# Performance work log

Measured on AMD Instinct MI355X. Metric: run time of the kernel, lower is better.

## Reference

```python
import jax, jax.numpy as jnp
import numpy as np

MIN_NORM = 1e-15
PROJ_EPS = 4e-3  # HGCN float32 boundary eps
C = 1.0          # curvature (all layers)
N_BRANCH = 4


def artanh(x):
    return jnp.arctanh(jnp.clip(x, -1.0 + 1e-7, 1.0 - 1e-7))


def _norm(x):
    return jnp.clip(jnp.linalg.norm(x, axis=-1, keepdims=True), MIN_NORM)


def proj(x, c):
    n = _norm(x)
    maxn = (1.0 - PROJ_EPS) / jnp.sqrt(c)
    return jnp.where(n > maxn, x / n * maxn, x)


def expmap0(u, c):
    sc = jnp.sqrt(c)
    n = _norm(u)
    return jnp.tanh(sc * n) * u / (sc * n)


def logmap0(p, c):
    sc = jnp.sqrt(c)
    n = _norm(p)
    return artanh(sc * n) * p / (sc * n)


def mobius_add(x, y, c):
    x2 = jnp.sum(x * x, -1, keepdims=True)
    y2 = jnp.sum(y * y, -1, keepdims=True)
    xy = jnp.sum(x * y, -1, keepdims=True)
    num = (1.0 + 2.0 * c * xy + c * y2) * x + (1.0 - c * x2) * y
    den = 1.0 + 2.0 * c * xy + c * c * x2 * y2
    return num / jnp.clip(den, MIN_NORM)


def mobius_matvec(W, x, c):
    sc = jnp.sqrt(c)
    xn = _norm(x)
    mx = x @ W.T
    mxn = _norm(mx)
    res = jnp.tanh(mxn / xn * artanh(sc * xn)) * mx / (mxn * sc)
    zero = jnp.all(mx == 0, axis=-1, keepdims=True)
    return jnp.where(zero, jnp.zeros((), x.dtype), res)


def mobius_mulscaler(r, x, c):
    sc = jnp.sqrt(c)
    xn = _norm(x)
    return jnp.tanh(r * artanh(sc * xn)) * x / (xn * sc)


def spmm(src, dst, w, xt, n):
    # out[i] = sum_{e: dst[e]=i} w[e] * xt[src[e]]
    return jax.ops.segment_sum(w[:, None] * xt[src], dst, num_segments=n)


def hgc_layer(h, W, b, src, dst, w, n):
    # HypLinear (dropout=0)
    h = proj(mobius_matvec(W, h, C), C)
    hb = proj(expmap0(b[None, :], C), C)
    h = proj(mobius_add(h, hb, C), C)
    # HypAgg: sparse propagation in tangent space
    st = spmm(src, dst, w, logmap0(h, C), n)
    h = proj(expmap0(st, C), C)
    # HypAct (relu)
    return proj(expmap0(jax.nn.relu(logmap0(h, C)), C), C)


def encode(x, W0, b0, W1, b1, src, dst, w, n):
    h = proj(expmap0(x, C), C)  # proj_tan0 is identity on Poincare ball
    h = hgc_layer(h, W0, b0, src, dst, w, n)
    h = hgc_layer(h, W1, b1, src, dst, w, n)
    return h


def setup_inputs() -> dict:
    key = jax.random.key(0)
    ks = jax.random.split(key, 8)
    N, F_IN, HID, DIM, E = 50000, 128, 128, 64, 1600000
    x = jax.random.normal(ks[0], (N, F_IN), jnp.float32)
    edge_src = jax.random.randint(ks[1], (E,), 0, N, jnp.int32)
    edge_dst = jax.random.randint(ks[2], (E,), 0, N, jnp.int32)
    # positive, roughly row-normalized edge weights (avg degree 32)
    edge_w = jax.random.uniform(ks[3], (N_BRANCH, E), jnp.float32) / 32.0
    W0 = jax.random.normal(ks[4], (N_BRANCH, HID, F_IN), jnp.float32) * 0.05
    b0 = jax.random.normal(ks[5], (N_BRANCH, HID), jnp.float32) * 0.01
    W1 = jax.random.normal(ks[6], (N_BRANCH, DIM, HID), jnp.float32) * 0.05
    b1 = jax.random.normal(ks[7], (N_BRANCH, DIM), jnp.float32) * 0.01
    return {"x": x, "edge_src": edge_src, "edge_dst": edge_dst, "edge_w": edge_w,
            "W0": W0, "b0": b0, "W1": W1, "b1": b1}


def reference(x, edge_src, edge_dst, edge_w, W0, b0, W1, b1):
    n = x.shape[0]
    # 4 directional-proximity branches (d_i, d_o, n_i, n_o); fixed small loop
    branches = [encode(x, W0[i], b0[i], W1[i], b1[i], edge_src, edge_dst, edge_w[i], n)
                for i in range(N_BRANCH)]
    # Mobius-weighted (scalar 1/8) combination, left-to-right mobius_add chain
    target = mobius_mulscaler(0.125, branches[0], C)
    for br in branches[1:]:
        target = mobius_add(target, mobius_mulscaler(0.125, br, C), C)
    feat = jnp.stack(branches + [target], axis=1)  # [N, 5, dim]
    # HypAttnAgg (use_att=False) with row-normalized per-node star adjacency:
    # target row of each 5-block = mean of the 5 tangent vectors
    agg = logmap0(feat, C).mean(axis=1)            # [N, dim]
    return proj(expmap0(agg, C), C)
```

## Files before the change

### kernel.cpp

```cpp
#include <hip/hip_runtime.h>
#include <math.h>

#define MAXN_P 0.996f

typedef unsigned short bfraw;
typedef __attribute__((ext_vector_type(8))) short bf16x8;
typedef __attribute__((ext_vector_type(4))) float f32x4;

__device__ __forceinline__ float wred(float v){
  #pragma unroll
  for(int o=32;o>0;o>>=1) v += __shfl_xor(v,o,64);
  return v;
}
template<int W>
__device__ __forceinline__ float gredw(float v){
  #pragma unroll
  for(int o=W/2;o>0;o>>=1) v += __shfl_xor(v,o,64);
  return v;
}
__device__ __forceinline__ float artanh_c(float x){
  x = fminf(fmaxf(x, -1.0f+1e-7f), 1.0f-1e-7f);
  return atanhf(x);
}
__device__ __forceinline__ float sel4(float4 w, int g){
  float ab = (g&1) ? w.y : w.x;
  float cd = (g&1) ? w.w : w.z;
  return (g&2) ? cd : ab;
}
__device__ __forceinline__ bfraw f2bf(float f){
  unsigned u = __float_as_uint(f);
  unsigned r = (u + 0x7fffu + ((u>>16)&1u)) >> 16;
  return (bfraw)r;
}
__device__ __forceinline__ float bflo(unsigned u){ return __uint_as_float(u<<16); }
__device__ __forceinline__ float bfhi(unsigned u){ return __uint_as_float(u & 0xffff0000u); }

__device__ __forceinline__ void acc8(float* a, float w, uint4 u){
  a[0]=fmaf(w, bflo(u.x), a[0]); a[1]=fmaf(w, bfhi(u.x), a[1]);
  a[2]=fmaf(w, bflo(u.y), a[2]); a[3]=fmaf(w, bfhi(u.y), a[3]);
  a[4]=fmaf(w, bflo(u.z), a[4]); a[5]=fmaf(w, bfhi(u.z), a[5]);
  a[6]=fmaf(w, bflo(u.w), a[6]); a[7]=fmaf(w, bfhi(u.w), a[7]);
}
__device__ __forceinline__ void acc4(float* a, float w, uint2 u){
  a[0]=fmaf(w, bflo(u.x), a[0]); a[1]=fmaf(w, bfhi(u.x), a[1]);
  a[2]=fmaf(w, bflo(u.y), a[2]); a[3]=fmaf(w, bfhi(u.y), a[3]);
}

template<int W, int K>
__device__ __forceinline__ float postK(const float* u, float* h){
  float ss = 0.f;
  #pragma unroll
  for(int k=0;k<K;k++) ss += u[k]*u[k];
  ss = gredw<W>(ss);
  float un = fmaxf(sqrtf(ss), 1e-15f);
  float t1 = tanhf(un);
  float sc = t1/un;
  float pn = t1;
  if (pn > MAXN_P){ sc *= MAXN_P/pn; pn = MAXN_P; }
  float ln = fmaxf(pn, 1e-15f);
  float m = sc * (artanh_c(ln)/ln);
  float v[K]; float vs = 0.f;
  #pragma unroll
  for(int k=0;k<K;k++){ v[k] = fmaxf(u[k]*m, 0.f); vs += v[k]*v[k]; }
  vs = gredw<W>(vs);
  float vn = fmaxf(sqrtf(vs), 1e-15f);
  float t2 = tanhf(vn);
  float qs = t2/vn;
  float qn = t2;
  if (qn > MAXN_P){ qs *= MAXN_P/qn; qn = MAXN_P; }
  #pragma unroll
  for(int k=0;k<K;k++) h[k] = v[k]*qs;
  return qn;
}

__global__ void k_hist(const int* __restrict__ dst, int* __restrict__ cnt, int E){
  int e = blockIdx.x*blockDim.x + threadIdx.x;
  if (e < E) atomicAdd(&cnt[dst[e]], 1);
}

__global__ void k_scan(const int* __restrict__ cnt, int* __restrict__ rowptr,
                       int* __restrict__ cursor, int N){
  __shared__ int sh[1024];
  int t = threadIdx.x;
  int chunk = (N + 1023) / 1024;
  int b = t*chunk;
  int e = b + chunk; if (e > N) e = N;
  int s = 0;
  for(int i=b;i<e && i<N;i++) s += cnt[i];
  sh[t] = s;
  __syncthreads();
  for(int off=1; off<1024; off<<=1){
    int add = (t>=off) ? sh[t-off] : 0;
    __syncthreads();
    sh[t] += add;
    __syncthreads();
  }
  int run = (t==0) ? 0 : sh[t-1];
  for(int i=b;i<e && i<N;i++){
    rowptr[i] = run; cursor[i] = run; run += cnt[i];
  }
  if (t == 1023) rowptr[N] = run;
}

__global__ void k_fill(const int* __restrict__ src, const int* __restrict__ dst,
                       const float* __restrict__ ew, int E,
                       int* __restrict__ cursor, int* __restrict__ srcs,
                       float4* __restrict__ wq){
  int e = blockIdx.x*blockDim.x + threadIdx.x;
  if (e >= E) return;
  int d = dst[e];
  int pos = atomicAdd(&cursor[d], 1);
  srcs[pos] = src[e];
  wq[pos] = make_float4(ew[e], ew[(size_t)E + e], ew[2*(size_t)E + e], ew[3*(size_t)E + e]);
}

__global__ void k_exp0(const float* __restrict__ x, bfraw* __restrict__ h0,
                       float* __restrict__ n0, int N){
  int wid = (blockIdx.x*blockDim.x + threadIdx.x)>>6;
  int lane = threadIdx.x & 63;
  if (wid >= N) return;
  const float* r = x + (size_t)wid*128;
  float u0 = r[lane], u1 = r[lane+64];
  float ss = wred(u0*u0 + u1*u1);
  float un = fmaxf(sqrtf(ss), 1e-15f);
  float tn = tanhf(un);
  float sc = tn/un;
  float pn = tn;
  if (pn > MAXN_P){ sc *= MAXN_P/pn; pn = MAXN_P; }
  h0[(size_t)wid*128 + lane]      = f2bf(u0*sc);
  h0[(size_t)wid*128 + lane + 64] = f2bf(u1*sc);
  if (lane == 0) n0[wid] = pn;
}

__global__ void k_hb(const float* __restrict__ b0, const float* __restrict__ b1,
                     float* __restrict__ hb0, float* __restrict__ hb1,
                     int HID, int DIM){
  int bl = blockIdx.x;
  int lane = threadIdx.x;
  int layer = bl >> 2, br = bl & 3;
  int D = layer ? DIM : HID;
  const float* b = layer ? (b1 + (size_t)br*DIM) : (b0 + (size_t)br*HID);
  float* o       = layer ? (hb1 + (size_t)br*DIM) : (hb0 + (size_t)br*HID);
  float v0 = (lane < D) ? b[lane] : 0.f;
  float v1 = (lane+64 < D) ? b[lane+64] : 0.f;
  float ss = wred(v0*v0 + v1*v1);
  float n = fmaxf(sqrtf(ss), 1e-15f);
  float tn = tanhf(n);
  float sc = tn/n;
  if (tn > MAXN_P) sc *= MAXN_P/tn;
  if (lane < D)    o[lane]    = v0*sc;
  if (lane+64 < D) o[lane+64] = v1*sc;
}

__global__ void k_w2bf(const float* __restrict__ a, bfraw* __restrict__ o, int n){
  int i = blockIdx.x*blockDim.x + threadIdx.x;
  if (i < n) o[i] = f2bf(a[i]);
}

template<int CT>
__global__ __launch_bounds__(256) void k_gemm_fused(
    const bfraw* __restrict__ Abase, int lda, int abroff,
    const bfraw* __restrict__ Wb,
    const float* __restrict__ nin, int nstride, int nbroff,
    const float* __restrict__ hball,
    bfraw* __restrict__ xt,
    int M)
{
  constexpr int BN = CT*16;
  __shared__ bfraw tile[64*BN];
  int br = blockIdx.z;
  const bfraw* A = Abase + (size_t)br*abroff;
  const bfraw* W = Wb + (size_t)br*BN*128;
  const float* hb = hball + (size_t)br*BN;
  int rb = blockIdx.x*64;
  int t = threadIdx.x;
  int wave = t>>6, lane = t&63;
  int cl = lane&15, grp = lane>>4;

  int rowA = rb + wave*16 + cl;
  bf16x8 afr[4];
  bf16x8 zf = {0,0,0,0,0,0,0,0};
  #pragma unroll
  for(int ks=0;ks<4;ks++){
    if (rowA < M) afr[ks] = *(const bf16x8*)(A + (size_t)rowA*lda + ks*32 + grp*8);
    else          afr[ks] = zf;
  }
  f32x4 acc[CT];
  #pragma unroll
  for(int ct=0;ct<CT;ct++) acc[ct] = f32x4{0.f,0.f,0.f,0.f};
  #pragma unroll
  for(int ct=0;ct<CT;ct++){
    #pragma unroll
    for(int ks=0;ks<4;ks++){
      bf16x8 bfr = *(const bf16x8*)(W + (size_t)(ct*16+cl)*128 + ks*32 + grp*8);
      acc[ct] = __builtin_amdgcn_mfma_f32_16x16x32_bf16(afr[ks], bfr, acc[ct], 0,0,0);
    }
  }
  float hv[CT]; float hb2 = 0.f;
  #pragma unroll
  for(int ct=0;ct<CT;ct++){ hv[ct] = hb[cl+16*ct]; hb2 += hv[ct]*hv[ct]; }
  hb2 = gredw<16>(hb2);
  #pragma unroll
  for(int j=0;j<4;j++){
    int rloc = wave*16 + grp*4 + j;
    int node = rb + rloc;
    bool v = node < M;
    float m[CT]; float ss = 0.f;
    #pragma unroll
    for(int ct=0;ct<CT;ct++){ m[ct] = acc[ct][j]; ss += m[ct]*m[ct]; }
    ss = gredw<16>(ss);
    float mxn_raw = sqrtf(ss);
    float mxn = fmaxf(mxn_raw, 1e-15f);
    float xn = fmaxf(v ? nin[(size_t)node*nstride + br*nbroff] : 1.f, 1e-15f);
    float th = tanhf(mxn/xn * artanh_c(xn));
    float hs = (mxn_raw > 0.f) ? th/mxn : 0.f;
    float hn = (mxn_raw > 0.f) ? th : 0.f;
    if (hn > MAXN_P){ hs *= MAXN_P/hn; hn = MAXN_P; }
    float h[CT]; float xy = 0.f, x2 = 0.f;
    #pragma unroll
    for(int ct=0;ct<CT;ct++){ h[ct] = m[ct]*hs; xy += h[ct]*hv[ct]; x2 += h[ct]*h[ct]; }
    xy = gredw<16>(xy); x2 = gredw<16>(x2);
    float c1 = 1.f + 2.f*xy + hb2;
    float c2 = 1.f - x2;
    float den = fmaxf(1.f + 2.f*xy + x2*hb2, 1e-15f);
    float a[CT]; float as = 0.f;
    #pragma unroll
    for(int ct=0;ct<CT;ct++){ a[ct] = (c1*h[ct] + c2*hv[ct])/den; as += a[ct]*a[ct]; }
    as = gredw<16>(as);
    float an = fmaxf(sqrtf(as), 1e-15f);
    float s2 = 1.f;
    if (an > MAXN_P){ s2 = MAXN_P/an; an = MAXN_P; }
    float ls = artanh_c(an)/an * s2;
    #pragma unroll
    for(int ct=0;ct<CT;ct++) tile[rloc*BN + cl + 16*ct] = f2bf(a[ct]*ls);
  }
  __syncthreads();
  constexpr int IT = (64*BN)/(256*8);
  #pragma unroll
  for(int i=0;i<IT;i++){
    int flat = (t + i*256)*8;
    int row = flat/BN, col = flat%BN;
    int node = rb + row;
    if (node < M)
      *(uint4*)(xt + ((size_t)node*4 + br)*BN + col) = *(const uint4*)(tile + row*BN + col);
  }
}

__global__ __launch_bounds__(256) void k_spmm_l0(const int* __restrict__ rowptr,
                        const int* __restrict__ srcs, const float4* __restrict__ wq,
                        const bfraw* __restrict__ xt,
                        bfraw* __restrict__ hout, float* __restrict__ n4, int N){
  int wid = (blockIdx.x*blockDim.x + threadIdx.x)>>6;
  int lane = threadIdx.x & 63;
  if (wid >= N) return;
  int g = lane>>4;
  float acc[8] = {0,0,0,0,0,0,0,0};
  int p0 = rowptr[wid], p1 = rowptr[wid+1];
  int p = p0;
  for (; p+4 <= p1; p += 4){
    int s0 = srcs[p], s1 = srcs[p+1], s2 = srcs[p+2], s3 = srcs[p+3];
    float4 w0 = wq[p], w1 = wq[p+1], w2 = wq[p+2], w3 = wq[p+3];
    uint4 u0 = *((const uint4*)(xt + (size_t)s0*512) + lane);
    uint4 u1 = *((const uint4*)(xt + (size_t)s1*512) + lane);
    uint4 u2 = *((const uint4*)(xt + (size_t)s2*512) + lane);
    uint4 u3 = *((const uint4*)(xt + (size_t)s3*512) + lane);
    acc8(acc, sel4(w0,g), u0);
    acc8(acc, sel4(w1,g), u1);
    acc8(acc, sel4(w2,g), u2);
    acc8(acc, sel4(w3,g), u3);
  }
  for (; p < p1; ++p){
    int s0 = srcs[p];
    float4 w0 = wq[p];
    uint4 u0 = *((const uint4*)(xt + (size_t)s0*512) + lane);
    acc8(acc, sel4(w0,g), u0);
  }
  float h[8];
  float qn = postK<16,8>(acc, h);
  uint4 o;
  o.x = (unsigned)f2bf(h[0]) | ((unsigned)f2bf(h[1])<<16);
  o.y = (unsigned)f2bf(h[2]) | ((unsigned)f2bf(h[3])<<16);
  o.z = (unsigned)f2bf(h[4]) | ((unsigned)f2bf(h[5])<<16);
  o.w = (unsigned)f2bf(h[6]) | ((unsigned)f2bf(h[7])<<16);
  *((uint4*)(hout + (size_t)wid*512) + lane) = o;
  if ((lane&15)==0) n4[(size_t)wid*4 + g] = qn;
}

__global__ __launch_bounds__(256) void k_spmm_l1(const int* __restrict__ rowptr,
                        const int* __restrict__ srcs, const float4* __restrict__ wq,
                        const bfraw* __restrict__ xt,
                        float* __restrict__ out, int N){
  int wid = (blockIdx.x*blockDim.x + threadIdx.x)>>6;
  int lane = threadIdx.x & 63;
  if (wid >= N) return;
  int g = lane>>4;
  int slot = lane & 15;
  float acc[4] = {0,0,0,0};
  int p0 = rowptr[wid], p1 = rowptr[wid+1];
  int p = p0;
  for (; p+4 <= p1; p += 4){
    int s0 = srcs[p], s1 = srcs[p+1], s2 = srcs[p+2], s3 = srcs[p+3];
    float4 w0 = wq[p], w1 = wq[p+1], w2 = wq[p+2], w3 = wq[p+3];
    uint2 u0 = *((const uint2*)(xt + (size_t)s0*256) + lane);
    uint2 u1 = *((const uint2*)(xt + (size_t)s1*256) + lane);
    uint2 u2 = *((const uint2*)(xt + (size_t)s2*256) + lane);
    uint2 u3 = *((const uint2*)(xt + (size_t)s3*256) + lane);
    acc4(acc, sel4(w0,g), u0);
    acc4(acc, sel4(w1,g), u1);
    acc4(acc, sel4(w2,g), u2);
    acc4(acc, sel4(w3,g), u3);
  }
  for (; p < p1; ++p){
    int s0 = srcs[p];
    float4 w0 = wq[p];
    uint2 u0 = *((const uint2*)(xt + (size_t)s0*256) + lane);
    acc4(acc, sel4(w0,g), u0);
  }
  float hv[4];
  float qn = postK<16,4>(acc, hv);
  float xk[4][4]; float qk[4];
  #pragma unroll
  for(int k=0;k<4;k++){
    #pragma unroll
    for(int j=0;j<4;j++) xk[k][j] = __shfl(hv[j], slot + 16*k, 64);
    qk[k] = __shfl(qn, 16*k, 64);
  }
  float xn0 = fmaxf(qk[0], 1e-15f);
  float s0 = tanhf(0.125f*artanh_c(xn0))/xn0;
  float t[4] = {s0*xk[0][0], s0*xk[0][1], s0*xk[0][2], s0*xk[0][3]};
  #pragma unroll
  for(int k=1;k<4;k++){
    float yn = fmaxf(qk[k], 1e-15f);
    float sy = tanhf(0.125f*artanh_c(yn))/yn;
    float y[4] = {sy*xk[k][0], sy*xk[k][1], sy*xk[k][2], sy*xk[k][3]};
    float dx=0.f, dy=0.f, dxy=0.f;
    #pragma unroll
    for(int j=0;j<4;j++){ dx += t[j]*t[j]; dy += y[j]*y[j]; dxy += t[j]*y[j]; }
    float x2 = gredw<16>(dx);
    float y2 = gredw<16>(dy);
    float xy = gredw<16>(dxy);
    float c1 = 1.f + 2.f*xy + y2;
    float c2 = 1.f - x2;
    float den = fmaxf(1.f + 2.f*xy + x2*y2, 1e-15f);
    #pragma unroll
    for(int j=0;j<4;j++) t[j] = (c1*t[j] + c2*y[j])/den;
  }
  float s[4] = {0,0,0,0};
  #pragma unroll
  for(int k=0;k<4;k++){
    float nk = fmaxf(qk[k], 1e-15f);
    float lk = artanh_c(nk)/nk;
    #pragma unroll
    for(int j=0;j<4;j++) s[j] = fmaf(lk, xk[k][j], s[j]);
  }
  float dt = 0.f;
  #pragma unroll
  for(int j=0;j<4;j++) dt += t[j]*t[j];
  float tn = fmaxf(sqrtf(gredw<16>(dt)), 1e-15f);
  float lt = artanh_c(tn)/tn;
  #pragma unroll
  for(int j=0;j<4;j++) s[j] = 0.2f*fmaf(lt, t[j], s[j]);
  float ds = 0.f;
  #pragma unroll
  for(int j=0;j<4;j++) ds += s[j]*s[j];
  float an = fmaxf(sqrtf(gredw<16>(ds)), 1e-15f);
  float on = tanhf(an);
  float osc = on/an;
  if (on > MAXN_P) osc *= MAXN_P/on;
  if (g == 0)
    *(float4*)(out + (size_t)wid*64 + 4*slot) =
      make_float4(s[0]*osc, s[1]*osc, s[2]*osc, s[3]*osc);
}

extern "C" void kernel_launch(void* const* d_in, const int* in_sizes, int n_in,
                              void* d_out, int out_size, void* d_ws, size_t ws_size,
                              hipStream_t stream){
  const float* x   = (const float*)d_in[0];
  const int*   src = (const int*)d_in[1];
  const int*   dst = (const int*)d_in[2];
  const float* ew  = (const float*)d_in[3];
  const float* W0  = (const float*)d_in[4];
  const float* b0  = (const float*)d_in[5];
  const float* W1  = (const float*)d_in[6];
  const float* b1  = (const float*)d_in[7];
  float* out = (float*)d_out;

  const int FIN = 128;
  int N = in_sizes[0]/FIN;
  int E = in_sizes[1];
  int HID = in_sizes[5]/4;
  int DIM = in_sizes[7]/4;

  char* ws = (char*)d_ws;
  size_t off = 0;
  auto alloc = [&](size_t bytes)->char*{
    char* p = ws + off;
    off += (bytes + 255) & ~(size_t)255;
    return p;
  };
  bfraw* h4b    = (bfraw*)alloc((size_t)N*4*FIN*2);
  bfraw* xtb    = (bfraw*)alloc((size_t)N*4*FIN*2);
  float* n0     = (float*)alloc((size_t)N*4);
  float* n4     = (float*)alloc((size_t)N*16);
  int*   rowptr = (int*)alloc((size_t)(N+1)*4);
  int*   cnt    = (int*)alloc((size_t)N*4);
  int*   cursor = (int*)alloc((size_t)N*4);
  int*   srcs   = (int*)alloc((size_t)E*4);
  float4* wq    = (float4*)alloc((size_t)E*16);
  float* hb0    = (float*)alloc((size_t)4*HID*4);
  float* hb1    = (float*)alloc((size_t)4*DIM*4);
  bfraw* w0b    = (bfraw*)alloc((size_t)4*HID*FIN*2);
  bfraw* w1b    = (bfraw*)alloc((size_t)4*DIM*HID*2);
  (void)ws_size; (void)n_in; (void)out_size;

  bfraw* h0 = h4b;

  int rowBlocks  = (N + 3)/4;

  hipMemsetAsync(cnt, 0, (size_t)N*4, stream);
  k_hist<<<(E+255)/256, 256, 0, stream>>>(dst, cnt, E);
  k_scan<<<1, 1024, 0, stream>>>(cnt, rowptr, cursor, N);
  k_fill<<<(E+255)/256, 256, 0, stream>>>(src, dst, ew, E, cursor, srcs, wq);

  k_exp0<<<rowBlocks, 256, 0, stream>>>(x, h0, n0, N);
  k_hb<<<8, 64, 0, stream>>>(b0, b1, hb0, hb1, HID, DIM);
  k_w2bf<<<(4*HID*FIN+255)/256, 256, 0, stream>>>(W0, w0b, 4*HID*FIN);
  k_w2bf<<<(4*DIM*HID+255)/256, 256, 0, stream>>>(W1, w1b, 4*DIM*HID);

  k_gemm_fused<8><<<dim3((N+63)/64, 1, 4), 256, 0, stream>>>(
      h0, FIN, 0, w0b, n0, 1, 0, hb0, xtb, N);
  k_spmm_l0<<<rowBlocks, 256, 0, stream>>>(rowptr, srcs, wq, xtb, h4b, n4, N);

  k_gemm_fused<4><<<dim3((N+63)/64, 1, 4), 256, 0, stream>>>(
      h4b, 4*HID, HID, w1b, n4, 4, 1, hb1, xtb, N);
  k_spmm_l1<<<rowBlocks, 256, 0, stream>>>(rowptr, srcs, wq, xtb, out, N);
}
```

Measured before the change: 812.9 us.

## Pack edge weights to fp16 and process two edges per wave in layer-1 SpMM

Edge weights for the four branches are stored as packed fp16 (8 bytes per edge) instead of float4 (16 bytes), halving the weight traffic in both SpMM passes and in the fill kernel. The layer-1 SpMM now splits the wave into two halves, each handling a different edge with 16-byte loads, and combines the halves with a cross-half shuffle. The Mobius combination epilogue is restructured to match the 8-lane groups. The cost is reduced edge-weight precision and a more complex lane mapping.

New measurement: 832.1 us. 1.02x slower.

```diff
diff --git a/kernel.cpp b/kernel.cpp
--- a/kernel.cpp
+++ b/kernel.cpp
@@ -21,11 +21,6 @@
 __device__ __forceinline__ float artanh_c(float x){
   x = fminf(fmaxf(x, -1.0f+1e-7f), 1.0f-1e-7f);
   return atanhf(x);
-}
-__device__ __forceinline__ float sel4(float4 w, int g){
-  float ab = (g&1) ? w.y : w.x;
-  float cd = (g&1) ? w.w : w.z;
-  return (g&2) ? cd : ab;
 }
 __device__ __forceinline__ bfraw f2bf(float f){
   unsigned u = __float_as_uint(f);
@@ -34,16 +29,24 @@
 }
 __device__ __forceinline__ float bflo(unsigned u){ return __uint_as_float(u<<16); }
 __device__ __forceinline__ float bfhi(unsigned u){ return __uint_as_float(u & 0xffff0000u); }
+
+__device__ __forceinline__ unsigned short f2h(float f){
+  _Float16 x = (_Float16)f; unsigned short h; __builtin_memcpy(&h, &x, 2); return h;
+}
+__device__ __forceinline__ float h2f(unsigned short h){
+  _Float16 f; __builtin_memcpy(&f, &h, 2); return (float)f;
+}
+__device__ __forceinline__ float wsel(uint2 w, bool g1, bool g2){
+  unsigned word = g2 ? w.y : w.x;
+  unsigned hu = g1 ? (word>>16) : (word & 0xffffu);
+  return h2f((unsigned short)hu);
+}
 
 __device__ __forceinline__ void acc8(float* a, float w, uint4 u){
   a[0]=fmaf(w, bflo(u.x), a[0]); a[1]=fmaf(w, bfhi(u.x), a[1]);
   a[2]=fmaf(w, bflo(u.y), a[2]); a[3]=fmaf(w, bfhi(u.y), a[3]);
   a[4]=fmaf(w, bflo(u.z), a[4]); a[5]=fmaf(w, bfhi(u.z), a[5]);
   a[6]=fmaf(w, bflo(u.w), a[6]); a[7]=fmaf(w, bfhi(u.w), a[7]);
-}
-__device__ __forceinline__ void acc4(float* a, float w, uint2 u){
-  a[0]=fmaf(w, bflo(u.x), a[0]); a[1]=fmaf(w, bfhi(u.x), a[1]);
-  a[2]=fmaf(w, bflo(u.y), a[2]); a[3]=fmaf(w, bfhi(u.y), a[3]);
 }
 
 template<int W, int K>
@@ -105,13 +108,17 @@
 __global__ void k_fill(const int* __restrict__ src, const int* __restrict__ dst,
                        const float* __restrict__ ew, int E,
                        int* __restrict__ cursor, int* __restrict__ srcs,
-                       float4* __restrict__ wq){
+                       uint2* __restrict__ wq2){
   int e = blockIdx.x*blockDim.x + threadIdx.x;
   if (e >= E) return;
   int d = dst[e];
   int pos = atomicAdd(&cursor[d], 1);
   srcs[pos] = src[e];
-  wq[pos] = make_float4(ew[e], ew[(size_t)E + e], ew[2*(size_t)E + e], ew[3*(size_t)E + e]);
+  unsigned h0 = f2h(ew[e]);
+  unsigned h1 = f2h(ew[(size_t)E + e]);
+  unsigned h2 = f2h(ew[2*(size_t)E + e]);
+  unsigned h3 = f2h(ew[3*(size_t)E + e]);
+  wq2[pos] = make_uint2(h0 | (h1<<16), h2 | (h3<<16));
 }
 
 __global__ void k_exp0(const float* __restrict__ x, bfraw* __restrict__ h0,
@@ -247,33 +254,34 @@
 }
 
 __global__ __launch_bounds__(256) void k_spmm_l0(const int* __restrict__ rowptr,
-                        const int* __restrict__ srcs, const float4* __restrict__ wq,
+                        const int* __restrict__ srcs, const uint2* __restrict__ wq2,
                         const bfraw* __restrict__ xt,
                         bfraw* __restrict__ hout, float* __restrict__ n4, int N){
   int wid = (blockIdx.x*blockDim.x + threadIdx.x)>>6;
   int lane = threadIdx.x & 63;
   if (wid >= N) return;
   int g = lane>>4;
+  bool g1 = (g&1)!=0, g2 = (g&2)!=0;
   float acc[8] = {0,0,0,0,0,0,0,0};
   int p0 = rowptr[wid], p1 = rowptr[wid+1];
   int p = p0;
   for (; p+4 <= p1; p += 4){
     int s0 = srcs[p], s1 = srcs[p+1], s2 = srcs[p+2], s3 = srcs[p+3];
-    float4 w0 = wq[p], w1 = wq[p+1], w2 = wq[p+2], w3 = wq[p+3];
+    uint2 w0 = wq2[p], w1 = wq2[p+1], w2 = wq2[p+2], w3 = wq2[p+3];
     uint4 u0 = *((const uint4*)(xt + (size_t)s0*512) + lane);
     uint4 u1 = *((const uint4*)(xt + (size_t)s1*512) + lane);
     uint4 u2 = *((const uint4*)(xt + (size_t)s2*512) + lane);
     uint4 u3 = *((const uint4*)(xt + (size_t)s3*512) + lane);
-    acc8(acc, sel4(w0,g), u0);
-    acc8(acc, sel4(w1,g), u1);
-    acc8(acc, sel4(w2,g), u2);
-    acc8(acc, sel4(w3,g), u3);
+    acc8(acc, wsel(w0,g1,g2), u0);
+    acc8(acc, wsel(w1,g1,g2), u1);
+    acc8(acc, wsel(w2,g1,g2), u2);
+    acc8(acc, wsel(w3,g1,g2), u3);
   }
   for (; p < p1; ++p){
     int s0 = srcs[p];
-    float4 w0 = wq[p];
+    uint2 w0 = wq2[p];
     uint4 u0 = *((const uint4*)(xt + (size_t)s0*512) + lane);
-    acc8(acc, sel4(w0,g), u0);
+    acc8(acc, wsel(w0,g1,g2), u0);
   }
   float h[8];
   float qn = postK<16,8>(acc, h);
@@ -287,89 +295,101 @@
 }
 
 __global__ __launch_bounds__(256) void k_spmm_l1(const int* __restrict__ rowptr,
-                        const int* __restrict__ srcs, const float4* __restrict__ wq,
+                        const int* __restrict__ srcs, const uint2* __restrict__ wq2,
                         const bfraw* __restrict__ xt,
                         float* __restrict__ out, int N){
   int wid = (blockIdx.x*blockDim.x + threadIdx.x)>>6;
   int lane = threadIdx.x & 63;
   if (wid >= N) return;
-  int g = lane>>4;
-  int slot = lane & 15;
-  float acc[4] = {0,0,0,0};
+  bool hi = lane >= 32;
+  int l31 = lane & 31;
+  int g = l31 >> 3;
+  bool g1 = (g&1)!=0, g2 = (g&2)!=0;
+  int slot = lane & 7;
+  float acc[8] = {0,0,0,0,0,0,0,0};
   int p0 = rowptr[wid], p1 = rowptr[wid+1];
   int p = p0;
-  for (; p+4 <= p1; p += 4){
-    int s0 = srcs[p], s1 = srcs[p+1], s2 = srcs[p+2], s3 = srcs[p+3];
-    float4 w0 = wq[p], w1 = wq[p+1], w2 = wq[p+2], w3 = wq[p+3];
-    uint2 u0 = *((const uint2*)(xt + (size_t)s0*256) + lane);
-    uint2 u1 = *((const uint2*)(xt + (size_t)s1*256) + lane);
-    uint2 u2 = *((const uint2*)(xt + (size_t)s2*256) + lane);
-    uint2 u3 = *((const uint2*)(xt + (size_t)s3*256) + lane);
-    acc4(acc, sel4(w0,g), u0);
-    acc4(acc, sel4(w1,g), u1);
-    acc4(acc, sel4(w2,g), u2);
-    acc4(acc, sel4(w3,g), u3);
-  }
-  for (; p < p1; ++p){
-    int s0 = srcs[p];
-    float4 w0 = wq[p];
-    uint2 u0 = *((const uint2*)(xt + (size_t)s0*256) + lane);
-    acc4(acc, sel4(w0,g), u0);
-  }
-  float hv[4];
-  float qn = postK<16,4>(acc, hv);
-  float xk[4][4]; float qk[4];
-  #pragma unroll
-  for(int k=0;k<4;k++){
-    #pragma unroll
-    for(int j=0;j<4;j++) xk[k][j] = __shfl(hv[j], slot + 16*k, 64);
-    qk[k] = __shfl(qn, 16*k, 64);
-  }
-  float xn0 = fmaxf(qk[0], 1e-15f);
-  float s0 = tanhf(0.125f*artanh_c(xn0))/xn0;
-  float t[4] = {s0*xk[0][0], s0*xk[0][1], s0*xk[0][2], s0*xk[0][3]};
+  for (; p+8 <= p1; p += 8){
+    uint4 u[4]; float wl[4];
+    #pragma unroll
+    for(int i=0;i<4;i++){
+      int sA = srcs[p+2*i], sB = srcs[p+2*i+1];
+      uint2 wA = wq2[p+2*i], wB = wq2[p+2*i+1];
+      int sE = hi ? sB : sA;
+      uint2 wE; wE.x = hi ? wB.x : wA.x; wE.y = hi ? wB.y : wA.y;
+      u[i] = *((const uint4*)(xt + (size_t)sE*256) + l31);
+      wl[i] = wsel(wE, g1, g2);
+    }
+    #pragma unroll
+    for(int i=0;i<4;i++) acc8(acc, wl[i], u[i]);
+  }
+  for (; p < p1; p += 2){
+    int sA = srcs[p];
+    bool hasB = (p+1 < p1);
+    int sB = hasB ? srcs[p+1] : sA;
+    uint2 wA = wq2[p];
+    uint2 wB = hasB ? wq2[p+1] : make_uint2(0u,0u);
+    int sE = hi ? sB : sA;
+    uint2 wE; wE.x = hi ? wB.x : wA.x; wE.y = hi ? wB.y : wA.y;
+    uint4 u = *((const uint4*)(xt + (size_t)sE*256) + l31);
+    acc8(acc, wsel(wE,g1,g2), u);
+  }
+  #pragma unroll
+  for(int k=0;k<8;k++) acc[k] += __shfl_xor(acc[k], 32, 64);
+  float h[8];
+  float qn = postK<8,8>(acc, h);
+  float t[8], s[8];
+  float qk0 = fmaxf(__shfl(qn, (lane&32) + 0, 64), 1e-15f);
+  float lk0 = artanh_c(qk0)/qk0;
+  float s0 = tanhf(0.125f*artanh_c(qk0))/qk0;
+  #pragma unroll
+  for(int j=0;j<8;j++){
+    float xv = __shfl(h[j], (lane&32) + slot, 64);
+    t[j] = s0*xv;
+    s[j] = lk0*xv;
+  }
   #pragma unroll
   for(int k=1;k<4;k++){
-    float yn = fmaxf(qk[k], 1e-15f);
-    float sy = tanhf(0.125f*artanh_c(yn))/yn;
-    float y[4] = {sy*xk[k][0], sy*xk[k][1], sy*xk[k][2], sy*xk[k][3]};
+    float qk = fmaxf(__shfl(qn, (lane&32) + k*8, 64), 1e-15f);
+    float lk = artanh_c(qk)/qk;
+    float sy = tanhf(0.125f*artanh_c(qk))/qk;
+    float y[8];
     float dx=0.f, dy=0.f, dxy=0.f;
     #pragma unroll
-    for(int j=0;j<4;j++){ dx += t[j]*t[j]; dy += y[j]*y[j]; dxy += t[j]*y[j]; }
-    float x2 = gredw<16>(dx);
-    float y2 = gredw<16>(dy);
-    float xy = gredw<16>(dxy);
+    for(int j=0;j<8;j++){
+      float xv = __shfl(h[j], (lane&32) + k*8 + slot, 64);
+      y[j] = sy*xv;
+      s[j] = fmaf(lk, xv, s[j]);
+      dx += t[j]*t[j]; dy += y[j]*y[j]; dxy += t[j]*y[j];
+    }
+    float x2 = gredw<8>(dx);
+    float y2 = gredw<8>(dy);
+    float xy = gredw<8>(dxy);
     float c1 = 1.f + 2.f*xy + y2;
     float c2 = 1.f - x2;
     float den = fmaxf(1.f + 2.f*xy + x2*y2, 1e-15f);
     #pragma unroll
-    for(int j=0;j<4;j++) t[j] = (c1*t[j] + c2*y[j])/den;
-  }
-  float s[4] = {0,0,0,0};
-  #pragma unroll
-  for(int k=0;k<4;k++){
-    float nk = fmaxf(qk[k], 1e-15f);
-    float lk = artanh_c(nk)/nk;
-    #pragma unroll
-    for(int j=0;j<4;j++) s[j] = fmaf(lk, xk[k][j], s[j]);
+    for(int j=0;j<8;j++) t[j] = (c1*t[j] + c2*y[j])/den;
   }
   float dt = 0.f;
   #pragma unroll
-  for(int j=0;j<4;j++) dt += t[j]*t[j];
-  float tn = fmaxf(sqrtf(gredw<16>(dt)), 1e-15f);
+  for(int j=0;j<8;j++) dt += t[j]*t[j];
+  float tn = fmaxf(sqrtf(gredw<8>(dt)), 1e-15f);
   float lt = artanh_c(tn)/tn;
   #pragma unroll
-  for(int j=0;j<4;j++) s[j] = 0.2f*fmaf(lt, t[j], s[j]);
+  for(int j=0;j<8;j++) s[j] = 0.2f*fmaf(lt, t[j], s[j]);
   float ds = 0.f;
   #pragma unroll
-  for(int j=0;j<4;j++) ds += s[j]*s[j];
-  float an = fmaxf(sqrtf(gredw<16>(ds)), 1e-15f);
+  for(int j=0;j<8;j++) ds += s[j]*s[j];
+  float an = fmaxf(sqrtf(gredw<8>(ds)), 1e-15f);
   float on = tanhf(an);
   float osc = on/an;
   if (on > MAXN_P) osc *= MAXN_P/on;
-  if (g == 0)
-    *(float4*)(out + (size_t)wid*64 + 4*slot) =
-      make_float4(s[0]*osc, s[1]*osc, s[2]*osc, s[3]*osc);
+  if (lane < 8){
+    float* orow = out + (size_t)wid*64 + slot*8;
+    *(float4*)(orow)     = make_float4(s[0]*osc, s[1]*osc, s[2]*osc, s[3]*osc);
+    *(float4*)(orow + 4) = make_float4(s[4]*osc, s[5]*osc, s[6]*osc, s[7]*osc);
+  }
 }
 
 extern "C" void kernel_launch(void* const* d_in, const int* in_sizes, int n_in,
@@ -406,7 +426,7 @@
   int*   cnt    = (int*)alloc((size_t)N*4);
   int*   cursor = (int*)alloc((size_t)N*4);
   int*   srcs   = (int*)alloc((size_t)E*4);
-  float4* wq    = (float4*)alloc((size_t)E*16);
+  uint2* wq2    = (uint2*)alloc((size_t)E*8);
   float* hb0    = (float*)alloc((size_t)4*HID*4);
   float* hb1    = (float*)alloc((size_t)4*DIM*4);
   bfraw* w0b    = (bfraw*)alloc((size_t)4*HID*FIN*2);
@@ -420,7 +440,7 @@
   hipMemsetAsync(cnt, 0, (size_t)N*4, stream);
   k_hist<<<(E+255)/256, 256, 0, stream>>>(dst, cnt, E);
   k_scan<<<1, 1024, 0, stream>>>(cnt, rowptr, cursor, N);
-  k_fill<<<(E+255)/256, 256, 0, stream>>>(src, dst, ew, E, cursor, srcs, wq);
+  k_fill<<<(E+255)/256, 256, 0, stream>>>(src, dst, ew, E, cursor, srcs, wq2);
 
   k_exp0<<<rowBlocks, 256, 0, stream>>>(x, h0, n0, N);
   k_hb<<<8, 64, 0, stream>>>(b0, b1, hb0, hb1, HID, DIM);
@@ -429,9 +449,9 @@
 
   k_gemm_fused<8><<<dim3((N+63)/64, 1, 4), 256, 0, stream>>>(
       h0, FIN, 0, w0b, n0, 1, 0, hb0, xtb, N);
-  k_spmm_l0<<<rowBlocks, 256, 0, stream>>>(rowptr, srcs, wq, xtb, h4b, n4, N);
+  k_spmm_l0<<<rowBlocks, 256, 0, stream>>>(rowptr, srcs, wq2, xtb, h4b, n4, N);
 
   k_gemm_fused<4><<<dim3((N+63)/64, 1, 4), 256, 0, stream>>>(
       h4b, 4*HID, HID, w1b, n4, 4, 1, hb1, xtb, N);
-  k_spmm_l1<<<rowBlocks, 256, 0, stream>>>(rowptr, srcs, wq, xtb, out, N);
-}
+  k_spmm_l1<<<rowBlocks, 256, 0, stream>>>(rowptr, srcs, wq2, xtb, out, N);
+}
```
